# Kernel tuning notes

Measured on AMD Instinct MI355X. Metric: run time of the kernel, lower is better.

Reference implementation:

```python
import jax, jax.numpy as jnp
import numpy as np

EPS = 1.1920929e-07  # torch F.rms_norm default eps (fp32 machine eps)
SOFTCAP = 30.0


def rmsnorm(x):
    return x * jax.lax.rsqrt(jnp.mean(x * x, axis=-1, keepdims=True) + EPS)


def prefix_matmul(M):
    # M: (B, T, k, 2, 2). Returns S with S[:, t] = M[:, t] @ M[:, t-1] @ ... @ M[:, 0].
    # associative combine: a precedes b in time, so combined = b @ a.
    return jax.lax.associative_scan(lambda a, b: jnp.matmul(b, a), M, axis=1)


def setup_inputs() -> dict:
    key = jax.random.key(0)
    ks = jax.random.split(key, 8)
    B, T, D, k, L, V = 32, 1024, 512, 128, 6, 2048
    return {
        "input_ids": jax.random.randint(ks[0], (B, T), 0, V),
        "target_ids": jax.random.randint(ks[1], (B, T), 0, V),
        "tok_emb": jax.random.normal(ks[2], (V, D), jnp.float32) * 0.005,
        "to_matrix_w": jax.random.normal(ks[3], (L, k * 4, D), jnp.float32) * 0.02,
        "v_vec": jax.random.normal(ks[4], (L, k, 2, 1), jnp.float32) * 0.02,
        "proj_w": jax.random.normal(ks[5], (L, D, k * 2), jnp.float32) * 0.02,
        "out_scale": jnp.ones((L, D), jnp.float32),
    }


def reference(input_ids, target_ids, tok_emb, to_matrix_w, v_vec, proj_w, out_scale):
    x = tok_emb[input_ids]                    # (B, T, D)
    x = rmsnorm(x)
    B, T, D = x.shape
    L = to_matrix_w.shape[0]
    k = to_matrix_w.shape[1] // 4
    for l in range(L):
        y = rmsnorm(x)
        M = jnp.einsum('btd,fd->btf', y, to_matrix_w[l]).reshape(B, T, k, 2, 2)
        n = jnp.sqrt(jnp.sum(M * M, axis=(-2, -1), keepdims=True))  # Frobenius norm
        M = M / jnp.maximum(n, 1e-6)
        S = prefix_matmul(M)                  # (B, T, k, 2, 2)
        h = jnp.matmul(S, v_vec[l]).squeeze(-1).reshape(B, T, k * 2)
        out = jnp.einsum('bth,dh->btd', h, proj_w[l])
        x = x + out_scale[l][None, None, :] * out
    x = rmsnorm(x)
    logits = jnp.einsum('btd,vd->btv', x, tok_emb)
    logits = SOFTCAP * jnp.tanh(logits / SOFTCAP)
    logp = jax.nn.log_softmax(logits.astype(jnp.float32).reshape(B * T, -1), axis=-1)
    tgt = target_ids.reshape(-1)
    loss = -jnp.mean(jnp.take_along_axis(logp, tgt[:, None], axis=1))
    return loss
```

## Files before the change

### kernel.cpp

```cpp
#include <hip/hip_runtime.h>
#include <math.h>

constexpr int NB = 32;
constexpr int NT = 1024;
constexpr int BT = 32768;
constexpr int DD = 512;
constexpr int KC = 128;
constexpr int NL = 6;
constexpr int NV = 2048;
constexpr int HH = 256;
constexpr int FF = 512;
constexpr int NC = NV / 128;
constexpr float EPS = 1.1920929e-07f;
constexpr float SOFTCAP = 30.0f;

typedef unsigned short u16;
typedef unsigned int u32;
using bf16x8 = __attribute__((ext_vector_type(8))) __bf16;
using f32x4 = __attribute__((ext_vector_type(4))) float;

__device__ __forceinline__ float wave_reduce_sum(float v) {
#pragma unroll
    for (int m = 32; m >= 1; m >>= 1) v += __shfl_xor(v, m, 64);
    return v;
}
__device__ __forceinline__ float wave_reduce_max(float v) {
#pragma unroll
    for (int m = 32; m >= 1; m >>= 1) v = fmaxf(v, __shfl_xor(v, m, 64));
    return v;
}

__device__ __forceinline__ u16 f2bf(float f) {
    u32 u = __float_as_uint(f);
    u = u + 0x7FFFu + ((u >> 16) & 1u);
    return (u16)(u >> 16);
}
__device__ __forceinline__ float bf2f(u16 v) {
    return __uint_as_float((u32)v << 16);
}

__device__ __forceinline__ float softcap30(float z) {
    float e = __expf(z * (2.0f / SOFTCAP));
    return SOFTCAP * (1.0f - 2.0f / (e + 1.0f));
}

__device__ __forceinline__ void gload_lds16(const void* gsrc, void* ldst) {
    __builtin_amdgcn_global_load_lds(
        (const __attribute__((address_space(1))) u32*)gsrc,
        (__attribute__((address_space(3))) u32*)ldst, 16, 0, 0);
}

__device__ __forceinline__ int2 swz_tile(int nbx, int nwg) {
    int bid = blockIdx.x;
    int cpx = nwg >> 3;
    int swz = (bid & 7) * cpx + (bid >> 3);
    return make_int2(swz % nbx, swz / nbx);
}

__global__ __launch_bounds__(256) void conv_bf_kernel(
        const float4* __restrict__ in, u16* __restrict__ out, int n4) {
    int i = blockIdx.x * 256 + threadIdx.x;
    if (i < n4) {
        float4 v = in[i];
        uint2 p;
        p.x = (u32)f2bf(v.x) | ((u32)f2bf(v.y) << 16);
        p.y = (u32)f2bf(v.z) | ((u32)f2bf(v.w) << 16);
        *(uint2*)(out + (size_t)i * 4) = p;
    }
}

__global__ __launch_bounds__(256) void embed_rms_kernel(
        const int* __restrict__ ids, const float* __restrict__ emb,
        float* __restrict__ x) {
    __shared__ float sw[4];
    int row = blockIdx.x;
    int id = ids[row];
    const float* e = emb + (size_t)id * DD;
    float* xo = x + (size_t)row * DD;
    int t = threadIdx.x;
    float v0 = e[t], v1 = e[t + 256];
    float ss = wave_reduce_sum(v0 * v0 + v1 * v1);
    if ((t & 63) == 0) sw[t >> 6] = ss;
    __syncthreads();
    ss = sw[0] + sw[1] + sw[2] + sw[3];
    float sc = rsqrtf(ss * (1.0f / DD) + EPS);
    xo[t] = v0 * sc;
    xo[t + 256] = v1 * sc;
}

__global__ __launch_bounds__(256) void ynorm_kernel(
        const float* __restrict__ x, u16* __restrict__ y,
        float* __restrict__ irms) {
    int lane = threadIdx.x & 63, wid = threadIdx.x >> 6;
    int row = blockIdx.x * 4 + wid;
    const float4* xr = (const float4*)(x + (size_t)row * DD);
    float4 a = xr[lane * 2], b = xr[lane * 2 + 1];
    float ss = a.x * a.x + a.y * a.y + a.z * a.z + a.w * a.w +
               b.x * b.x + b.y * b.y + b.z * b.z + b.w * b.w;
    ss = wave_reduce_sum(ss);
    float sc = rsqrtf(ss * (1.0f / DD) + EPS);
    u32 p0 = (u32)f2bf(a.x * sc) | ((u32)f2bf(a.y * sc) << 16);
    u32 p1 = (u32)f2bf(a.z * sc) | ((u32)f2bf(a.w * sc) << 16);
    u32 p2 = (u32)f2bf(b.x * sc) | ((u32)f2bf(b.y * sc) << 16);
    u32 p3 = (u32)f2bf(b.z * sc) | ((u32)f2bf(b.w * sc) << 16);
    *(uint4*)(y + (size_t)row * DD + lane * 8) = make_uint4(p0, p1, p2, p3);
    if (lane == 0) irms[row] = sc;
}

template <int MODE>
__global__ __launch_bounds__(256) void gemm_mfma_kernel(
        const u16* __restrict__ A, const u16* __restrict__ B,
        float* __restrict__ C, u16* __restrict__ Cb, int nbx, int nwg, int N,
        int K, const float* __restrict__ dscale, float* __restrict__ pm,
        float* __restrict__ ps) {
    __shared__ __align__(16) u16 As[128 * 32];
    __shared__ __align__(16) u16 Bs[128 * 32];
    int2 tc = swz_tile(nbx, nwg);
    int tx = tc.x, ty = tc.y;
    int tid = threadIdx.x;
    int lane = tid & 63, wid = tid >> 6;
    int wr = wid >> 1, wc = wid & 1;
    int m0 = ty * 128, n0 = tx * 128;
    const u16* Ag = A + (size_t)m0 * K;
    const u16* Bg = B + (size_t)n0 * K;
    int r0 = tid >> 2;
    int k8 = (tid & 3) * 8;
    int rl = lane & 15;
    int kk = (lane >> 4) * 8;
    f32x4 zero4 = {0.f, 0.f, 0.f, 0.f};
    f32x4 acc[4][4];
#pragma unroll
    for (int m = 0; m < 4; ++m)
#pragma unroll
        for (int n = 0; n < 4; ++n) acc[m][n] = zero4;

    int nk = K >> 5;
    for (int kt = 0; kt < nk; ++kt) {
        int kb = (kt << 5) + k8;
        __syncthreads();
        gload_lds16(Ag + (size_t)r0 * K + kb, &As[tid * 8]);
        gload_lds16(Ag + (size_t)(r0 + 64) * K + kb, &As[(tid + 256) * 8]);
        gload_lds16(Bg + (size_t)r0 * K + kb, &Bs[tid * 8]);
        gload_lds16(Bg + (size_t)(r0 + 64) * K + kb, &Bs[(tid + 256) * 8]);
        __syncthreads();
        bf16x8 af[4], bfr[4];
#pragma unroll
        for (int m = 0; m < 4; ++m)
            af[m] = *(const bf16x8*)&As[(wr * 64 + m * 16 + rl) * 32 + kk];
#pragma unroll
        for (int n = 0; n < 4; ++n)
            bfr[n] = *(const bf16x8*)&Bs[(wc * 64 + n * 16 + rl) * 32 + kk];
#pragma unroll
        for (int m = 0; m < 4; ++m)
#pragma unroll
            for (int n = 0; n < 4; ++n)
                acc[m][n] = __builtin_amdgcn_mfma_f32_16x16x32_bf16(
                    af[m], bfr[n], acc[m][n], 0, 0, 0);
    }

    int cr = (lane >> 4) * 4;
    int cc = lane & 15;
    if constexpr (MODE == 0) {
#pragma unroll
        for (int m = 0; m < 4; ++m)
#pragma unroll
            for (int n = 0; n < 4; ++n)
#pragma unroll
                for (int r = 0; r < 4; ++r) {
                    int row = m0 + wr * 64 + m * 16 + cr + r;
                    int col = n0 + wc * 64 + n * 16 + cc;
                    Cb[(size_t)row * N + col] = f2bf(acc[m][n][r]);
                }
    } else if constexpr (MODE == 1) {
        float ds[4];
#pragma unroll
        for (int n = 0; n < 4; ++n) ds[n] = dscale[n0 + wc * 64 + n * 16 + cc];
#pragma unroll
        for (int m = 0; m < 4; ++m)
#pragma unroll
            for (int n = 0; n < 4; ++n)
#pragma unroll
                for (int r = 0; r < 4; ++r) {
                    int row = m0 + wr * 64 + m * 16 + cr + r;
                    int col = n0 + wc * 64 + n * 16 + cc;
                    C[(size_t)row * N + col] += ds[n] * acc[m][n][r];
                }
    } else {
        __shared__ float redm[128][2];
        __shared__ float redsum[128][2];
#pragma unroll
        for (int m = 0; m < 4; ++m)
#pragma unroll
            for (int n = 0; n < 4; ++n)
#pragma unroll
                for (int r = 0; r < 4; ++r)
                    acc[m][n][r] = softcap30(acc[m][n][r]);
#pragma unroll
        for (int m = 0; m < 4; ++m)
#pragma unroll
            for (int r = 0; r < 4; ++r) {
                float lm = fmaxf(fmaxf(acc[m][0][r], acc[m][1][r]),
                                 fmaxf(acc[m][2][r], acc[m][3][r]));
                lm = fmaxf(lm, __shfl_xor(lm, 1, 64));
                lm = fmaxf(lm, __shfl_xor(lm, 2, 64));
                lm = fmaxf(lm, __shfl_xor(lm, 4, 64));
                lm = fmaxf(lm, __shfl_xor(lm, 8, 64));
                if (cc == 0) redm[wr * 64 + m * 16 + cr + r][wc] = lm;
            }
        __syncthreads();
#pragma unroll
        for (int m = 0; m < 4; ++m)
#pragma unroll
            for (int r = 0; r < 4; ++r) {
                int rowb = wr * 64 + m * 16 + cr + r;
                float bm = fmaxf(redm[rowb][0], redm[rowb][1]);
                float s = __expf(acc[m][0][r] - bm) + __expf(acc[m][1][r] - bm) +
                          __expf(acc[m][2][r] - bm) + __expf(acc[m][3][r] - bm);
                s += __shfl_xor(s, 1, 64);
                s += __shfl_xor(s, 2, 64);
                s += __shfl_xor(s, 4, 64);
                s += __shfl_xor(s, 8, 64);
                if (cc == 0) redsum[rowb][wc] = s;
            }
        __syncthreads();
        if (tid < 128) {
            float bm = fmaxf(redm[tid][0], redm[tid][1]);
            pm[(size_t)(m0 + tid) * NC + tx] = bm;
            ps[(size_t)(m0 + tid) * NC + tx] = redsum[tid][0] + redsum[tid][1];
        }
    }
}

__device__ __forceinline__ void mstep(ushort4 mv, float& S00, float& S01,
                                      float& S10, float& S11) {
    float e0 = bf2f(mv.x), e1 = bf2f(mv.y), e2 = bf2f(mv.z), e3 = bf2f(mv.w);
    float n2 = e0 * e0 + e1 * e1 + e2 * e2 + e3 * e3;
    float inv = 1.0f / fmaxf(sqrtf(n2), 1e-6f);
    float a00 = e0 * inv, a01 = e1 * inv, a10 = e2 * inv, a11 = e3 * inv;
    float t00 = a00 * S00 + a01 * S10;
    float t01 = a00 * S01 + a01 * S11;
    float t10 = a10 * S00 + a11 * S10;
    float t11 = a10 * S01 + a11 * S11;
    S00 = t00; S01 = t01; S10 = t10; S11 = t11;
}

__global__ __launch_bounds__(256) void scan_seg_kernel(
        const ushort4* __restrict__ Mh, float4* __restrict__ P) {
    int c = threadIdx.x & 127;
    int seg = ((blockIdx.x & 15) << 1) | (threadIdx.x >> 7);
    int b = blockIdx.x >> 4;
    size_t base = ((size_t)b * NT + seg * 32) * KC + c;
    float S00 = 1.f, S01 = 0.f, S10 = 0.f, S11 = 0.f;
#pragma unroll 4
    for (int u = 0; u < 32; ++u)
        mstep(Mh[base + (size_t)u * KC], S00, S01, S10, S11);
    P[((size_t)b * 32 + seg) * KC + c] = make_float4(S00, S01, S10, S11);
}

__global__ __launch_bounds__(256) void scan_exc_kernel(
        const float4* __restrict__ P, float4* __restrict__ E) {
    int g = blockIdx.x * 256 + threadIdx.x;
    int b = g >> 7, c = g & 127;
    float S00 = 1.f, S01 = 0.f, S10 = 0.f, S11 = 0.f;
    for (int s = 0; s < 32; ++s) {
        size_t idx = ((size_t)b * 32 + s) * KC + c;
        E[idx] = make_float4(S00, S01, S10, S11);
        float4 p = P[idx];
        float t00 = p.x * S00 + p.y * S10;
        float t01 = p.x * S01 + p.y * S11;
        float t10 = p.z * S00 + p.w * S10;
        float t11 = p.z * S01 + p.w * S11;
        S00 = t00; S01 = t01; S10 = t10; S11 = t11;
    }
}

__global__ __launch_bounds__(256) void scan_apply_kernel(
        const ushort4* __restrict__ Mh, const float4* __restrict__ E,
        const float* __restrict__ vv, ushort2* __restrict__ h2) {
    int c = threadIdx.x & 127;
    int seg = ((blockIdx.x & 15) << 1) | (threadIdx.x >> 7);
    int b = blockIdx.x >> 4;
    float4 e = E[((size_t)b * 32 + seg) * KC + c];
    float S00 = e.x, S01 = e.y, S10 = e.z, S11 = e.w;
    float v0 = vv[c * 2], v1 = vv[c * 2 + 1];
    size_t base = ((size_t)b * NT + seg * 32) * KC + c;
#pragma unroll 4
    for (int u = 0; u < 32; ++u) {
        mstep(Mh[base + (size_t)u * KC], S00, S01, S10, S11);
        float h0 = S00 * v0 + S01 * v1;
        float h1 = S10 * v0 + S11 * v1;
        h2[base + (size_t)u * KC] = make_ushort2(f2bf(h0), f2bf(h1));
    }
}

__global__ __launch_bounds__(256) void loss_stage2_kernel(
        const float* __restrict__ x, const float* __restrict__ irms,
        const float* __restrict__ emb, const int* __restrict__ tgt,
        const float* __restrict__ pm, const float* __restrict__ ps,
        float* __restrict__ rl) {
    int lane = threadIdx.x & 63, wid = threadIdx.x >> 6;
    int row = blockIdx.x * 4 + wid;
    float pmv = (lane < NC) ? pm[(size_t)row * NC + lane] : -3.0e38f;
    float m = wave_reduce_max(pmv);
    float s = (lane < NC) ? ps[(size_t)row * NC + lane] * __expf(pmv - m) : 0.f;
    s = wave_reduce_sum(s);
    float lse = m + __logf(s);
    int t = tgt[row];
    const float* xr = x + (size_t)row * DD;
    const float* er = emb + (size_t)t * DD;
    float z = 0.f;
#pragma unroll
    for (int d = lane; d < DD; d += 64) z += xr[d] * er[d];
    z = wave_reduce_sum(z) * irms[row];
    if (lane == 0) rl[row] = lse - softcap30(z);
}

__global__ __launch_bounds__(1024) void finalize_kernel(
        const float* __restrict__ rl, float* __restrict__ out) {
    __shared__ float sw[16];
    float s = 0.f;
    for (int i = threadIdx.x; i < BT; i += 1024) s += rl[i];
    s = wave_reduce_sum(s);
    if ((threadIdx.x & 63) == 0) sw[threadIdx.x >> 6] = s;
    __syncthreads();
    if (threadIdx.x == 0) {
        float t = 0.f;
#pragma unroll
        for (int i = 0; i < 16; ++i) t += sw[i];
        out[0] = t * (1.0f / BT);
    }
}

extern "C" void kernel_launch(void* const* d_in, const int* in_sizes, int n_in,
                              void* d_out, int out_size, void* d_ws,
                              size_t ws_size, hipStream_t stream) {
    (void)in_sizes; (void)n_in; (void)out_size; (void)ws_size;
    const int* ids = (const int*)d_in[0];
    const int* tgt = (const int*)d_in[1];
    const float* emb = (const float*)d_in[2];
    const float* Wm = (const float*)d_in[3];
    const float* vv = (const float*)d_in[4];
    const float* Pw = (const float*)d_in[5];
    const float* osc = (const float*)d_in[6];
    float* out = (float*)d_out;

    float* x = (float*)d_ws;
    u16* y = (u16*)(x + (size_t)BT * DD);
    u16* Mbh = y + (size_t)BT * DD;
    u16* hbf = Mbh + (size_t)BT * FF;
    float* P = (float*)(hbf + (size_t)BT * HH);
    float* E = P + (size_t)4096 * 32 * 4;
    float* irms = E + (size_t)4096 * 32 * 4;
    float* pm = irms + BT;
    float* ps = pm + (size_t)BT * NC;
    float* rl = ps + (size_t)BT * NC;
    u16* WmBf = (u16*)(rl + BT);
    u16* PwBf = WmBf + (size_t)NL * FF * DD;
    u16* embBf = PwBf + (size_t)NL * DD * HH;

    conv_bf_kernel<<<1536, 256, 0, stream>>>((const float4*)Wm, WmBf,
                                             NL * FF * DD / 4);
    conv_bf_kernel<<<768, 256, 0, stream>>>((const float4*)Pw, PwBf,
                                            NL * DD * HH / 4);
    conv_bf_kernel<<<1024, 256, 0, stream>>>((const float4*)emb, embBf,
                                             NV * DD / 4);
    embed_rms_kernel<<<BT, 256, 0, stream>>>(ids, emb, x);

    for (int l = 0; l < NL; ++l) {
        ynorm_kernel<<<BT / 4, 256, 0, stream>>>(x, y, irms);
        gemm_mfma_kernel<0><<<(FF / 128) * (BT / 128), 256, 0, stream>>>(
            y, WmBf + (size_t)l * FF * DD, nullptr, Mbh, FF / 128,
            (FF / 128) * (BT / 128), FF, DD, nullptr, nullptr, nullptr);
        scan_seg_kernel<<<512, 256, 0, stream>>>((const ushort4*)Mbh,
                                                 (float4*)P);
        scan_exc_kernel<<<16, 256, 0, stream>>>((const float4*)P, (float4*)E);
        scan_apply_kernel<<<512, 256, 0, stream>>>(
            (const ushort4*)Mbh, (const float4*)E, vv + l * HH, (ushort2*)hbf);
        gemm_mfma_kernel<1><<<(DD / 128) * (BT / 128), 256, 0, stream>>>(
            hbf, PwBf + (size_t)l * DD * HH, x, nullptr, DD / 128,
            (DD / 128) * (BT / 128), DD, HH, osc + (size_t)l * DD, nullptr,
            nullptr);
    }

    ynorm_kernel<<<BT / 4, 256, 0, stream>>>(x, y, irms);
    gemm_mfma_kernel<2><<<(NV / 128) * (BT / 128), 256, 0, stream>>>(
        y, embBf, nullptr, nullptr, NV / 128, (NV / 128) * (BT / 128), NV, DD,
        nullptr, pm, ps);
    loss_stage2_kernel<<<BT / 4, 256, 0, stream>>>(x, irms, emb, tgt, pm, ps,
                                                   rl);
    finalize_kernel<<<1, 1024, 0, stream>>>(rl, out);
}
```

Before: 1.048 ms.

## Fuse three-pass scan into one LDS kernel, double-buffer GEMM, vectorize embed

The three scan kernels (segment products, exclusive prefix, apply) become one kernel per batch and 8-channel group. It stages M tiles in swizzled LDS, does a 64-lane shuffle-based prefix over 16-step segments, and writes h back coalesced through LDS. This removes two launches, the P/E workspace round trips and the repeated read of M. The GEMM gains a double-buffered LDS pipeline with one barrier per k-step and a k-chunk-major LDS layout. The embed kernel also changes to one wave per row with float4 access.

```diff
diff --git a/kernel.cpp b/kernel.cpp
--- a/kernel.cpp
+++ b/kernel.cpp
@@ -72,20 +72,20 @@
 __global__ __launch_bounds__(256) void embed_rms_kernel(
         const int* __restrict__ ids, const float* __restrict__ emb,
         float* __restrict__ x) {
-    __shared__ float sw[4];
-    int row = blockIdx.x;
+    int lane = threadIdx.x & 63, wid = threadIdx.x >> 6;
+    int row = blockIdx.x * 4 + wid;
     int id = ids[row];
-    const float* e = emb + (size_t)id * DD;
-    float* xo = x + (size_t)row * DD;
-    int t = threadIdx.x;
-    float v0 = e[t], v1 = e[t + 256];
-    float ss = wave_reduce_sum(v0 * v0 + v1 * v1);
-    if ((t & 63) == 0) sw[t >> 6] = ss;
-    __syncthreads();
-    ss = sw[0] + sw[1] + sw[2] + sw[3];
+    const float4* e = (const float4*)(emb + (size_t)id * DD);
+    float4 a = e[lane * 2], b = e[lane * 2 + 1];
+    float ss = a.x * a.x + a.y * a.y + a.z * a.z + a.w * a.w +
+               b.x * b.x + b.y * b.y + b.z * b.z + b.w * b.w;
+    ss = wave_reduce_sum(ss);
     float sc = rsqrtf(ss * (1.0f / DD) + EPS);
-    xo[t] = v0 * sc;
-    xo[t + 256] = v1 * sc;
+    a.x *= sc; a.y *= sc; a.z *= sc; a.w *= sc;
+    b.x *= sc; b.y *= sc; b.z *= sc; b.w *= sc;
+    float4* xo = (float4*)(x + (size_t)row * DD);
+    xo[lane * 2] = a;
+    xo[lane * 2 + 1] = b;
 }
 
 __global__ __launch_bounds__(256) void ynorm_kernel(
@@ -113,20 +113,20 @@
         float* __restrict__ C, u16* __restrict__ Cb, int nbx, int nwg, int N,
         int K, const float* __restrict__ dscale, float* __restrict__ pm,
         float* __restrict__ ps) {
-    __shared__ __align__(16) u16 As[128 * 32];
-    __shared__ __align__(16) u16 Bs[128 * 32];
+    __shared__ __align__(16) u16 As[2][4096];
+    __shared__ __align__(16) u16 Bs[2][4096];
     int2 tc = swz_tile(nbx, nwg);
     int tx = tc.x, ty = tc.y;
     int tid = threadIdx.x;
     int lane = tid & 63, wid = tid >> 6;
     int wr = wid >> 1, wc = wid & 1;
     int m0 = ty * 128, n0 = tx * 128;
-    const u16* Ag = A + (size_t)m0 * K;
-    const u16* Bg = B + (size_t)n0 * K;
-    int r0 = tid >> 2;
-    int k8 = (tid & 3) * 8;
+    int srow = tid & 127;
+    int sc8 = (tid >> 7) * 8;
+    const u16* Arow = A + (size_t)(m0 + srow) * K + sc8;
+    const u16* Brow = B + (size_t)(n0 + srow) * K + sc8;
     int rl = lane & 15;
-    int kk = (lane >> 4) * 8;
+    int fc = (lane >> 4) * 1024;
     f32x4 zero4 = {0.f, 0.f, 0.f, 0.f};
     f32x4 acc[4][4];
 #pragma unroll
@@ -134,28 +134,36 @@
 #pragma unroll
         for (int n = 0; n < 4; ++n) acc[m][n] = zero4;
 
+    auto stage = [&](int buf, int kt) {
+        int kb = kt << 5;
+        gload_lds16(Arow + kb, &As[buf][tid * 8]);
+        gload_lds16(Arow + kb + 16, &As[buf][(tid + 256) * 8]);
+        gload_lds16(Brow + kb, &Bs[buf][tid * 8]);
+        gload_lds16(Brow + kb + 16, &Bs[buf][(tid + 256) * 8]);
+    };
+
     int nk = K >> 5;
+    stage(0, 0);
+    int cur = 0;
     for (int kt = 0; kt < nk; ++kt) {
-        int kb = (kt << 5) + k8;
         __syncthreads();
-        gload_lds16(Ag + (size_t)r0 * K + kb, &As[tid * 8]);
-        gload_lds16(Ag + (size_t)(r0 + 64) * K + kb, &As[(tid + 256) * 8]);
-        gload_lds16(Bg + (size_t)r0 * K + kb, &Bs[tid * 8]);
-        gload_lds16(Bg + (size_t)(r0 + 64) * K + kb, &Bs[(tid + 256) * 8]);
-        __syncthreads();
+        if (kt + 1 < nk) stage(cur ^ 1, kt + 1);
+        const u16* Ap = &As[cur][fc + rl * 8];
+        const u16* Bp = &Bs[cur][fc + rl * 8];
         bf16x8 af[4], bfr[4];
 #pragma unroll
         for (int m = 0; m < 4; ++m)
-            af[m] = *(const bf16x8*)&As[(wr * 64 + m * 16 + rl) * 32 + kk];
+            af[m] = *(const bf16x8*)(Ap + (wr * 64 + m * 16) * 8);
 #pragma unroll
         for (int n = 0; n < 4; ++n)
-            bfr[n] = *(const bf16x8*)&Bs[(wc * 64 + n * 16 + rl) * 32 + kk];
+            bfr[n] = *(const bf16x8*)(Bp + (wc * 64 + n * 16) * 8);
 #pragma unroll
         for (int m = 0; m < 4; ++m)
 #pragma unroll
             for (int n = 0; n < 4; ++n)
                 acc[m][n] = __builtin_amdgcn_mfma_f32_16x16x32_bf16(
                     af[m], bfr[n], acc[m][n], 0, 0, 0);
+        cur ^= 1;
     }
 
     int cr = (lane >> 4) * 4;
@@ -244,52 +252,71 @@
     S00 = t00; S01 = t01; S10 = t10; S11 = t11;
 }
 
-__global__ __launch_bounds__(256) void scan_seg_kernel(
-        const ushort4* __restrict__ Mh, float4* __restrict__ P) {
-    int c = threadIdx.x & 127;
-    int seg = ((blockIdx.x & 15) << 1) | (threadIdx.x >> 7);
-    int b = blockIdx.x >> 4;
-    size_t base = ((size_t)b * NT + seg * 32) * KC + c;
+__global__ __launch_bounds__(512) void scan_fused_kernel(
+        const ushort4* __restrict__ Mh, const float* __restrict__ vv,
+        ushort2* __restrict__ h2) {
+    __shared__ ushort4 ms[8192];
+    int tid = threadIdx.x;
+    int bb = blockIdx.x >> 4;
+    int cg = (blockIdx.x & 15) * 8;
+    size_t gbase = (size_t)bb * NT * KC + cg;
+#pragma unroll
+    for (int i = 0; i < 16; ++i) {
+        int flat = i * 512 + tid;
+        int t = flat >> 3, cl = flat & 7;
+        int idx = ((cl << 10) | t) ^ ((t >> 4) & 15) ^ (cl << 1);
+        ms[idx] = Mh[gbase + (size_t)t * KC + cl];
+    }
+    __syncthreads();
+    int cl = tid >> 6;
+    int s = tid & 63;
+    ushort4 mreg[16];
+#pragma unroll
+    for (int u = 0; u < 16; ++u) {
+        int t = s * 16 + u;
+        int idx = ((cl << 10) | t) ^ ((t >> 4) & 15) ^ (cl << 1);
+        mreg[u] = ms[idx];
+    }
     float S00 = 1.f, S01 = 0.f, S10 = 0.f, S11 = 0.f;
-#pragma unroll 4
-    for (int u = 0; u < 32; ++u)
-        mstep(Mh[base + (size_t)u * KC], S00, S01, S10, S11);
-    P[((size_t)b * 32 + seg) * KC + c] = make_float4(S00, S01, S10, S11);
-}
-
-__global__ __launch_bounds__(256) void scan_exc_kernel(
-        const float4* __restrict__ P, float4* __restrict__ E) {
-    int g = blockIdx.x * 256 + threadIdx.x;
-    int b = g >> 7, c = g & 127;
-    float S00 = 1.f, S01 = 0.f, S10 = 0.f, S11 = 0.f;
-    for (int s = 0; s < 32; ++s) {
-        size_t idx = ((size_t)b * 32 + s) * KC + c;
-        E[idx] = make_float4(S00, S01, S10, S11);
-        float4 p = P[idx];
-        float t00 = p.x * S00 + p.y * S10;
-        float t01 = p.x * S01 + p.y * S11;
-        float t10 = p.z * S00 + p.w * S10;
-        float t11 = p.z * S01 + p.w * S11;
-        S00 = t00; S01 = t01; S10 = t10; S11 = t11;
-    }
-}
-
-__global__ __launch_bounds__(256) void scan_apply_kernel(
-        const ushort4* __restrict__ Mh, const float4* __restrict__ E,
-        const float* __restrict__ vv, ushort2* __restrict__ h2) {
-    int c = threadIdx.x & 127;
-    int seg = ((blockIdx.x & 15) << 1) | (threadIdx.x >> 7);
-    int b = blockIdx.x >> 4;
-    float4 e = E[((size_t)b * 32 + seg) * KC + c];
-    float S00 = e.x, S01 = e.y, S10 = e.z, S11 = e.w;
-    float v0 = vv[c * 2], v1 = vv[c * 2 + 1];
-    size_t base = ((size_t)b * NT + seg * 32) * KC + c;
-#pragma unroll 4
-    for (int u = 0; u < 32; ++u) {
-        mstep(Mh[base + (size_t)u * KC], S00, S01, S10, S11);
+#pragma unroll
+    for (int u = 0; u < 16; ++u) mstep(mreg[u], S00, S01, S10, S11);
+#pragma unroll
+    for (int d = 1; d < 64; d <<= 1) {
+        float b00 = __shfl_up(S00, d, 64);
+        float b01 = __shfl_up(S01, d, 64);
+        float b10 = __shfl_up(S10, d, 64);
+        float b11 = __shfl_up(S11, d, 64);
+        if (s >= d) {
+            float t00 = S00 * b00 + S01 * b10;
+            float t01 = S00 * b01 + S01 * b11;
+            float t10 = S10 * b00 + S11 * b10;
+            float t11 = S10 * b01 + S11 * b11;
+            S00 = t00; S01 = t01; S10 = t10; S11 = t11;
+        }
+    }
+    float E00 = __shfl_up(S00, 1, 64), E01 = __shfl_up(S01, 1, 64);
+    float E10 = __shfl_up(S10, 1, 64), E11 = __shfl_up(S11, 1, 64);
+    if (s == 0) { E00 = 1.f; E01 = 0.f; E10 = 0.f; E11 = 0.f; }
+    float v0 = vv[(cg + cl) * 2], v1 = vv[(cg + cl) * 2 + 1];
+    __syncthreads();
+    ushort2* hs = (ushort2*)ms;
+    S00 = E00; S01 = E01; S10 = E10; S11 = E11;
+#pragma unroll
+    for (int u = 0; u < 16; ++u) {
+        mstep(mreg[u], S00, S01, S10, S11);
         float h0 = S00 * v0 + S01 * v1;
         float h1 = S10 * v0 + S11 * v1;
-        h2[base + (size_t)u * KC] = make_ushort2(f2bf(h0), f2bf(h1));
+        int t = s * 16 + u;
+        int idx = ((cl << 10) | t) ^ ((((t >> 4) & 15) << 1)) ^ (cl << 2);
+        hs[idx] = make_ushort2(f2bf(h0), f2bf(h1));
+    }
+    __syncthreads();
+#pragma unroll
+    for (int i = 0; i < 16; ++i) {
+        int flat = i * 512 + tid;
+        int t = flat >> 3, c2 = flat & 7;
+        int idx = ((c2 << 10) | t) ^ ((((t >> 4) & 15) << 1)) ^ (c2 << 2);
+        h2[gbase + (size_t)t * KC + c2] = hs[idx];
     }
 }
 
@@ -348,9 +375,7 @@
     u16* y = (u16*)(x + (size_t)BT * DD);
     u16* Mbh = y + (size_t)BT * DD;
     u16* hbf = Mbh + (size_t)BT * FF;
-    float* P = (float*)(hbf + (size_t)BT * HH);
-    float* E = P + (size_t)4096 * 32 * 4;
-    float* irms = E + (size_t)4096 * 32 * 4;
+    float* irms = (float*)(hbf + (size_t)BT * HH);
     float* pm = irms + BT;
     float* ps = pm + (size_t)BT * NC;
     float* rl = ps + (size_t)BT * NC;
@@ -364,18 +389,15 @@
                                             NL * DD * HH / 4);
     conv_bf_kernel<<<1024, 256, 0, stream>>>((const float4*)emb, embBf,
                                              NV * DD / 4);
-    embed_rms_kernel<<<BT, 256, 0, stream>>>(ids, emb, x);
+    embed_rms_kernel<<<BT / 4, 256, 0, stream>>>(ids, emb, x);
 
     for (int l = 0; l < NL; ++l) {
         ynorm_kernel<<<BT / 4, 256, 0, stream>>>(x, y, irms);
         gemm_mfma_kernel<0><<<(FF / 128) * (BT / 128), 256, 0, stream>>>(
             y, WmBf + (size_t)l * FF * DD, nullptr, Mbh, FF / 128,
             (FF / 128) * (BT / 128), FF, DD, nullptr, nullptr, nullptr);
-        scan_seg_kernel<<<512, 256, 0, stream>>>((const ushort4*)Mbh,
-                                                 (float4*)P);
-        scan_exc_kernel<<<16, 256, 0, stream>>>((const float4*)P, (float4*)E);
-        scan_apply_kernel<<<512, 256, 0, stream>>>(
-            (const ushort4*)Mbh, (const float4*)E, vv + l * HH, (ushort2*)hbf);
+        scan_fused_kernel<<<NB * 16, 512, 0, stream>>>(
+            (const ushort4*)Mbh, vv + l * HH, (ushort2*)hbf);
         gemm_mfma_kernel<1><<<(DD / 128) * (BT / 128), 256, 0, stream>>>(
             hbf, PwBf + (size_t)l * DD * HH, x, nullptr, DD / 128,
             (DD / 128) * (BT / 128), DD, HH, osc + (size_t)l * DD, nullptr,
```

Result: slower. 1.193 ms (+13.8%).
